# Optimization experiments

Measured on AMD Instinct MI355X. Metric: run time of the kernel, lower is better.

## Reference

```python
import jax, jax.numpy as jnp
import numpy as np
import math

IN_FEATURES = 3072
PADDED = 4096  # next power of two
ACT_BITS = 8
LN_EPS = 1e-6


def hadamard_transform(x):
    """Normalized fast Walsh-Hadamard transform along last dim (power of 2)."""
    n = x.shape[-1]
    m = n.bit_length() - 1  # log2(n)
    shape = x.shape
    y = x.reshape(shape[:-1] + (2,) * m)
    for ax in range(len(shape) - 1, len(shape) - 1 + m):
        a = jnp.take(y, 0, axis=ax)
        b = jnp.take(y, 1, axis=ax)
        y = jnp.stack([a + b, a - b], axis=ax)
    return y.reshape(shape) / jnp.sqrt(jnp.asarray(n, x.dtype))


def activation_quant(x, bits=ACT_BITS):
    """Per-token absmax int-b quant with STE (BitNet style)."""
    qb = 2 ** (bits - 1) - 1  # 127
    scale = qb / jnp.clip(jnp.max(jnp.abs(x), axis=-1, keepdims=True), 1e-5)
    q = jnp.clip(jnp.round(x * scale), -qb - 1, qb) / scale
    return x + jax.lax.stop_gradient(q - x)


def weight_quant(w):
    """Ternary absmean weight quant with STE (as in training path)."""
    scale = jnp.clip(jnp.mean(jnp.abs(w)), 1e-5)
    q = jnp.clip(jnp.round(w / scale), -1.0, 1.0) * scale
    return w + jax.lax.stop_gradient(q - w)


def layer_norm(x, gamma, beta, eps=LN_EPS):
    mu = jnp.mean(x, axis=-1, keepdims=True)
    var = jnp.mean(jnp.square(x - mu), axis=-1, keepdims=True)
    return (x - mu) * jax.lax.rsqrt(var + eps) * gamma + beta


def setup_inputs() -> dict:
    key = jax.random.key(0)
    k1, k2 = jax.random.split(key)
    x = jax.random.normal(k1, (4, 2048, IN_FEATURES), dtype=jnp.float32)
    ln_gamma = jnp.ones((IN_FEATURES,), dtype=jnp.float32)
    ln_beta = jnp.zeros((IN_FEATURES,), dtype=jnp.float32)
    weight = jax.random.normal(k2, (4096, PADDED), dtype=jnp.float32) * 0.02
    return {"x": x, "ln_gamma": ln_gamma, "ln_beta": ln_beta, "weight": weight}


def reference(x, ln_gamma, ln_beta, weight):
    x_norm = layer_norm(x, ln_gamma, ln_beta)
    pad = PADDED - IN_FEATURES
    x_pad = jnp.pad(x_norm, ((0, 0), (0, 0), (0, pad)))
    x_had = hadamard_transform(x_pad)
    x_q = activation_quant(x_had)
    w_q = weight_quant(weight)
    # F.linear: x @ W^T
    out = jnp.einsum('bsd,od->bso', x_q, w_q)
    return out
```

## Files before the change

kernel.cpp:

```cpp
#include <hip/hip_runtime.h>
#include <stdint.h>

#define TOKENS 8192
#define IN_F   3072
#define PAD_F  4096
#define N_OUT  4096
#define K_DIM  4096

using i32x4 = __attribute__((ext_vector_type(4))) int;

#define Q_OFF    0
#define WQ_OFF   33554432
#define AINV_OFF 50331648
#define PART_OFF 50364416
#define WSC_OFF  50380800

__device__ __forceinline__ void gload_lds16(const void* g, void* l) {
    __builtin_amdgcn_global_load_lds(
        (__attribute__((address_space(1))) void*)(void*)g,
        (__attribute__((address_space(3))) void*)l,
        16, 0, 0);
}

__global__ __launch_bounds__(256) void k_wabs(const float* __restrict__ w,
                                              float* __restrict__ partial) {
    int tid = threadIdx.x;
    const float4* w4 = (const float4*)(w + (size_t)blockIdx.x * 4096);
    float s = 0.f;
#pragma unroll
    for (int i = 0; i < 4; ++i) {
        float4 v = w4[tid + i * 256];
        s += fabsf(v.x) + fabsf(v.y) + fabsf(v.z) + fabsf(v.w);
    }
#pragma unroll
    for (int o = 32; o > 0; o >>= 1) s += __shfl_xor(s, o);
    __shared__ float rb[4];
    if ((tid & 63) == 0) rb[tid >> 6] = s;
    __syncthreads();
    if (tid == 0) partial[blockIdx.x] = rb[0] + rb[1] + rb[2] + rb[3];
}

__global__ __launch_bounds__(256) void k_wscale(const float* __restrict__ partial,
                                                float* __restrict__ wsp) {
    int tid = threadIdx.x;
    float s = 0.f;
#pragma unroll
    for (int i = 0; i < 16; ++i) s += partial[tid + i * 256];
#pragma unroll
    for (int o = 32; o > 0; o >>= 1) s += __shfl_xor(s, o);
    __shared__ float rb[4];
    if ((tid & 63) == 0) rb[tid >> 6] = s;
    __syncthreads();
    if (tid == 0)
        wsp[0] = fmaxf((rb[0] + rb[1] + rb[2] + rb[3]) * (1.0f / 16777216.0f), 1e-5f);
}

__global__ __launch_bounds__(256) void k_wquant(const float* __restrict__ w,
                                                const float* __restrict__ wsp,
                                                unsigned int* __restrict__ wq) {
    int idx = blockIdx.x * 256 + threadIdx.x;
    float ws = wsp[0];
    float4 v = ((const float4*)w)[idx];
    int a = (int)rintf(v.x / ws); a = max(-1, min(1, a));
    int b = (int)rintf(v.y / ws); b = max(-1, min(1, b));
    int c = (int)rintf(v.z / ws); c = max(-1, min(1, c));
    int d = (int)rintf(v.w / ws); d = max(-1, min(1, d));
    unsigned int p = (unsigned)(a & 255) | ((unsigned)(b & 255) << 8) |
                     ((unsigned)(c & 255) << 16) | ((unsigned)(d & 255) << 24);
    wq[idx] = p;
}

__global__ __launch_bounds__(256) void k_lnfwht(const float* __restrict__ x,
                                                const float* __restrict__ gamma,
                                                const float* __restrict__ beta,
                                                signed char* __restrict__ q,
                                                float* __restrict__ ainv) {
    __shared__ float s[PAD_F];
    __shared__ float rb[8];
    int tid = threadIdx.x;
    int lane = tid & 63;
    int t = blockIdx.x;
    const float* xr = x + (size_t)t * IN_F;

    float v[16];
    float sum = 0.f;
#pragma unroll
    for (int i = 0; i < 12; ++i) { v[i] = xr[tid + i * 256]; sum += v[i]; }
    v[12] = v[13] = v[14] = v[15] = 0.f;
#pragma unroll
    for (int o = 32; o > 0; o >>= 1) sum += __shfl_xor(sum, o);
    if ((tid & 63) == 0) rb[tid >> 6] = sum;
    __syncthreads();
    float mu = (rb[0] + rb[1] + rb[2] + rb[3]) * (1.0f / 3072.0f);

    float s2 = 0.f;
#pragma unroll
    for (int i = 0; i < 12; ++i) { float d = v[i] - mu; s2 += d * d; }
#pragma unroll
    for (int o = 32; o > 0; o >>= 1) s2 += __shfl_xor(s2, o);
    if ((tid & 63) == 0) rb[4 + (tid >> 6)] = s2;
    __syncthreads();
    float var = (rb[4] + rb[5] + rb[6] + rb[7]) * (1.0f / 3072.0f);
    float rstd = 1.0f / sqrtf(var + 1e-6f);

#pragma unroll
    for (int i = 0; i < 12; ++i)
        v[i] = (v[i] - mu) * rstd * gamma[tid + i * 256] + beta[tid + i * 256];

#pragma unroll
    for (int b = 1; b < 16; b <<= 1) {
#pragma unroll
        for (int i = 0; i < 16; ++i) {
            if (!(i & b)) {
                float a0 = v[i], b0 = v[i | b];
                v[i] = a0 + b0;
                v[i | b] = a0 - b0;
            }
        }
    }
#pragma unroll
    for (int m = 1; m <= 32; m <<= 1) {
#pragma unroll
        for (int i = 0; i < 16; ++i) {
            float p = __shfl_xor(v[i], m);
            v[i] = (lane & m) ? (p - v[i]) : (v[i] + p);
        }
    }
#pragma unroll
    for (int m = 64; m <= 128; m <<= 1) {
        __syncthreads();
#pragma unroll
        for (int i = 0; i < 16; ++i) s[tid + i * 256] = v[i];
        __syncthreads();
#pragma unroll
        for (int i = 0; i < 16; ++i) {
            float p = s[(tid ^ m) + i * 256];
            v[i] = (tid & m) ? (p - v[i]) : (v[i] + p);
        }
    }

    float mx = 0.f;
#pragma unroll
    for (int i = 0; i < 16; ++i) mx = fmaxf(mx, fabsf(v[i]));
#pragma unroll
    for (int o = 32; o > 0; o >>= 1) mx = fmaxf(mx, __shfl_xor(mx, o));
    __syncthreads();
    if ((tid & 63) == 0) rb[tid >> 6] = mx;
    __syncthreads();
    float amraw = fmaxf(fmaxf(rb[0], rb[1]), fmaxf(rb[2], rb[3]));
    float amax = fmaxf(amraw * (1.0f / 64.0f), 1e-5f);
    float scale = 127.0f / amax;
    if (tid == 0) ainv[t] = amax * (1.0f / 127.0f);

    signed char* qr = q + (size_t)t * PAD_F;
#pragma unroll
    for (int i = 0; i < 16; ++i) {
        int qi = (int)rintf(v[i] * (1.0f / 64.0f) * scale);
        qi = max(-128, min(127, qi));
        qr[tid + i * 256] = (signed char)qi;
    }
}

#define BK 64
#define NT (K_DIM / BK)

__global__ __launch_bounds__(512, 2) void k_gemm(const signed char* __restrict__ Aq,
                                                 const signed char* __restrict__ Wq,
                                                 const float* __restrict__ ainv,
                                                 const float* __restrict__ wsp,
                                                 float* __restrict__ out) {
    __shared__ signed char sA[4][256 * BK];
    __shared__ signed char sB[4][256 * BK];

    int tid = threadIdx.x;
    int lane = tid & 63, wid = tid >> 6;

    int bid = blockIdx.x;
    int xcd = bid & 7, li = bid >> 3;
    int bmb = xcd * 4 + (li & 3);
    int bnb = li >> 2;
    size_t bm0 = (size_t)bmb * 256, bn0 = (size_t)bnb * 256;

    int wm = wid >> 2, wn = wid & 3;
    int lrow = lane & 15, hi = lane >> 4;

    int srow = lane >> 2;
    int schunk = (lane & 3) ^ ((lane >> 3) & 3);
    const signed char* gA = Aq + (bm0 + (size_t)(wid * 32 + srow)) * K_DIM + schunk * 16;
    const signed char* gB = Wq + (bn0 + (size_t)(wid * 32 + srow)) * K_DIM + schunk * 16;

    i32x4 acc[8][4];
#pragma unroll
    for (int m = 0; m < 8; ++m)
#pragma unroll
        for (int n = 0; n < 4; ++n) acc[m][n] = (i32x4){0, 0, 0, 0};

    int kx = hi ^ ((lane >> 1) & 3);
    int abase = (wm * 128 + lrow) * 4 + kx;
    int bbase = (wn * 64 + lrow) * 4 + kx;

    auto STAGE = [&](int b, int t) {
        size_t k0 = (size_t)t * BK;
        gload_lds16(gA + k0, &sA[b][(wid * 32) * BK]);
        gload_lds16(gA + k0 + (size_t)16 * K_DIM, &sA[b][(wid * 32 + 16) * BK]);
        gload_lds16(gB + k0, &sB[b][(wid * 32) * BK]);
        gload_lds16(gB + k0 + (size_t)16 * K_DIM, &sB[b][(wid * 32 + 16) * BK]);
    };

    auto COMPUTE = [&](int b) {
        const i32x4* va = (const i32x4*)&sA[b][0];
        const i32x4* vb = (const i32x4*)&sB[b][0];
        i32x4 af[8], bf[4];
#pragma unroll
        for (int m = 0; m < 8; ++m) af[m] = va[abase + m * 64];
#pragma unroll
        for (int n = 0; n < 4; ++n) bf[n] = vb[bbase + n * 64];
        __builtin_amdgcn_s_setprio(1);
#pragma unroll
        for (int m = 0; m < 8; ++m)
#pragma unroll
            for (int n = 0; n < 4; ++n)
                acc[m][n] = __builtin_amdgcn_mfma_i32_16x16x64_i8(af[m], bf[n], acc[m][n], 0, 0, 0);
        __builtin_amdgcn_s_setprio(0);
    };

    STAGE(0, 0);
    STAGE(1, 1);
    STAGE(2, 2);

#pragma unroll 1
    for (int t = 0; t < NT - 3; ++t) {
        STAGE((t + 3) & 3, t + 3);
        asm volatile("s_waitcnt vmcnt(12)" ::: "memory");
        __builtin_amdgcn_s_barrier();
        __builtin_amdgcn_sched_barrier(0);
        COMPUTE(t & 3);
        __builtin_amdgcn_sched_barrier(0);
        __builtin_amdgcn_s_barrier();
    }
    asm volatile("s_waitcnt vmcnt(8)" ::: "memory");
    __builtin_amdgcn_s_barrier();
    __builtin_amdgcn_sched_barrier(0);
    COMPUTE((NT - 3) & 3);
    asm volatile("s_waitcnt vmcnt(4)" ::: "memory");
    __builtin_amdgcn_s_barrier();
    __builtin_amdgcn_sched_barrier(0);
    COMPUTE((NT - 2) & 3);
    asm volatile("s_waitcnt vmcnt(0)" ::: "memory");
    __builtin_amdgcn_s_barrier();
    __builtin_amdgcn_sched_barrier(0);
    COMPUTE((NT - 1) & 3);

    float wsc = wsp[0];
#pragma unroll
    for (int m = 0; m < 8; ++m) {
        size_t row0 = bm0 + wm * 128 + m * 16 + hi * 4;
#pragma unroll
        for (int r = 0; r < 4; ++r) {
            size_t row = row0 + r;
            float sa = wsc * ainv[row];
#pragma unroll
            for (int n = 0; n < 4; ++n) {
                size_t col = bn0 + wn * 64 + n * 16 + lrow;
                out[row * N_OUT + col] = (float)acc[m][n][r] * sa;
            }
        }
    }
}

extern "C" void kernel_launch(void* const* d_in, const int* in_sizes, int n_in,
                              void* d_out, int out_size, void* d_ws, size_t ws_size,
                              hipStream_t stream) {
    const float* x     = (const float*)d_in[0];
    const float* gamma = (const float*)d_in[1];
    const float* beta  = (const float*)d_in[2];
    const float* w     = (const float*)d_in[3];
    float* out = (float*)d_out;
    char* ws = (char*)d_ws;

    signed char* q   = (signed char*)(ws + Q_OFF);
    signed char* wq  = (signed char*)(ws + WQ_OFF);
    float* ainv      = (float*)(ws + AINV_OFF);
    float* partial   = (float*)(ws + PART_OFF);
    float* wsp       = (float*)(ws + WSC_OFF);

    k_wabs<<<dim3(4096), dim3(256), 0, stream>>>(w, partial);
    k_wscale<<<dim3(1), dim3(256), 0, stream>>>(partial, wsp);
    k_wquant<<<dim3(16384), dim3(256), 0, stream>>>(w, wsp, (unsigned int*)wq);
    k_lnfwht<<<dim3(TOKENS), dim3(256), 0, stream>>>(x, gamma, beta, q, ainv);
    k_gemm<<<dim3(512), dim3(512), 0, stream>>>(q, wq, ainv, wsp, out);
}
```

Baseline: 244.8 us.

## Switch GEMM to 32x32x32 int8 MFMA with register double-buffered LDS fragments

Replaces the 16x16x64 int8 MFMA tiling with 32x32x32 instructions, which cuts the number of LDS fragment loads per output. It also adds register double-buffering: fragments for the next K-tile are read from LDS while the current tile's MFMAs run, and one barrier per iteration is removed. The loop is unrolled by two to alternate the fragment buffers, and the epilogue is remapped to the 32x32 accumulator layout. This raises register pressure and tightens the waitcnt and barrier ordering, so correctness depends on the reduced sync still protecting LDS buffer reuse.

```diff
diff --git a/kernel.cpp b/kernel.cpp
--- a/kernel.cpp
+++ b/kernel.cpp
@@ -7,7 +7,8 @@
 #define N_OUT  4096
 #define K_DIM  4096
 
-using i32x4 = __attribute__((ext_vector_type(4))) int;
+using i32x4  = __attribute__((ext_vector_type(4))) int;
+using i32x16 = __attribute__((ext_vector_type(16))) int;
 
 #define Q_OFF    0
 #define WQ_OFF   33554432
@@ -182,22 +183,24 @@
     size_t bm0 = (size_t)bmb * 256, bn0 = (size_t)bnb * 256;
 
     int wm = wid >> 2, wn = wid & 3;
-    int lrow = lane & 15, hi = lane >> 4;
 
     int srow = lane >> 2;
     int schunk = (lane & 3) ^ ((lane >> 3) & 3);
     const signed char* gA = Aq + (bm0 + (size_t)(wid * 32 + srow)) * K_DIM + schunk * 16;
     const signed char* gB = Wq + (bn0 + (size_t)(wid * 32 + srow)) * K_DIM + schunk * 16;
 
-    i32x4 acc[8][4];
-#pragma unroll
-    for (int m = 0; m < 8; ++m)
-#pragma unroll
-        for (int n = 0; n < 4; ++n) acc[m][n] = (i32x4){0, 0, 0, 0};
-
-    int kx = hi ^ ((lane >> 1) & 3);
-    int abase = (wm * 128 + lrow) * 4 + kx;
-    int bbase = (wn * 64 + lrow) * 4 + kx;
+    int r32 = lane & 31, ks32 = lane >> 5;
+    int kq = ks32 ^ ((r32 >> 1) & 3);
+    int abase = (wm * 128 + r32) * 4;
+    int bbase = (wn * 64 + r32) * 4;
+
+    i32x16 acc[4][2];
+#pragma unroll
+    for (int mf = 0; mf < 4; ++mf)
+#pragma unroll
+        for (int nf = 0; nf < 2; ++nf) acc[mf][nf] = (i32x16)(0);
+
+    i32x4 afA[2][4], bfA[2][2], afB[2][4], bfB[2][2];
 
     auto STAGE = [&](int b, int t) {
         size_t k0 = (size_t)t * BK;
@@ -207,65 +210,98 @@
         gload_lds16(gB + k0 + (size_t)16 * K_DIM, &sB[b][(wid * 32 + 16) * BK]);
     };
 
-    auto COMPUTE = [&](int b) {
-        const i32x4* va = (const i32x4*)&sA[b][0];
-        const i32x4* vb = (const i32x4*)&sB[b][0];
-        i32x4 af[8], bf[4];
-#pragma unroll
-        for (int m = 0; m < 8; ++m) af[m] = va[abase + m * 64];
-#pragma unroll
-        for (int n = 0; n < 4; ++n) bf[n] = vb[bbase + n * 64];
-        __builtin_amdgcn_s_setprio(1);
-#pragma unroll
-        for (int m = 0; m < 8; ++m)
-#pragma unroll
-            for (int n = 0; n < 4; ++n)
-                acc[m][n] = __builtin_amdgcn_mfma_i32_16x16x64_i8(af[m], bf[n], acc[m][n], 0, 0, 0);
-        __builtin_amdgcn_s_setprio(0);
-    };
+#define LOADF(B, AF, BF) do {                                           \
+    const i32x4* va = (const i32x4*)&sA[B][0];                          \
+    const i32x4* vb = (const i32x4*)&sB[B][0];                          \
+    _Pragma("unroll")                                                   \
+    for (int ks = 0; ks < 2; ++ks) {                                    \
+        int kx = (ks << 1) ^ kq;                                        \
+        _Pragma("unroll")                                               \
+        for (int mf = 0; mf < 4; ++mf) AF[ks][mf] = va[abase + mf * 128 + kx]; \
+        _Pragma("unroll")                                               \
+        for (int nf = 0; nf < 2; ++nf) BF[ks][nf] = vb[bbase + nf * 128 + kx]; \
+    }                                                                   \
+} while (0)
+
+#define COMPUTE(AF, BF) do {                                            \
+    __builtin_amdgcn_s_setprio(1);                                      \
+    _Pragma("unroll")                                                   \
+    for (int ks = 0; ks < 2; ++ks)                                      \
+        _Pragma("unroll")                                               \
+        for (int mf = 0; mf < 4; ++mf)                                  \
+            _Pragma("unroll")                                           \
+            for (int nf = 0; nf < 2; ++nf)                              \
+                acc[mf][nf] = __builtin_amdgcn_mfma_i32_32x32x32_i8(    \
+                    AF[ks][mf], BF[ks][nf], acc[mf][nf], 0, 0, 0);      \
+    __builtin_amdgcn_s_setprio(0);                                      \
+} while (0)
+
+#define BODY(T, AFC, BFC, AFN, BFN) do {                                \
+    STAGE((T + 3) & 3, T + 3);                                          \
+    asm volatile("s_waitcnt vmcnt(8)" ::: "memory");                    \
+    __builtin_amdgcn_sched_barrier(0);                                  \
+    __builtin_amdgcn_s_barrier();                                       \
+    __builtin_amdgcn_sched_barrier(0);                                  \
+    LOADF((T + 1) & 3, AFN, BFN);                                       \
+    COMPUTE(AFC, BFC);                                                  \
+    asm volatile("s_waitcnt lgkmcnt(0)" ::: "memory");                  \
+    __builtin_amdgcn_sched_barrier(0);                                  \
+} while (0)
 
     STAGE(0, 0);
     STAGE(1, 1);
     STAGE(2, 2);
+    asm volatile("s_waitcnt vmcnt(8)" ::: "memory");
+    __builtin_amdgcn_sched_barrier(0);
+    __builtin_amdgcn_s_barrier();
+    __builtin_amdgcn_sched_barrier(0);
+    LOADF(0, afA, bfA);
+    asm volatile("s_waitcnt lgkmcnt(0)" ::: "memory");
+    __builtin_amdgcn_sched_barrier(0);
 
 #pragma unroll 1
-    for (int t = 0; t < NT - 3; ++t) {
-        STAGE((t + 3) & 3, t + 3);
-        asm volatile("s_waitcnt vmcnt(12)" ::: "memory");
-        __builtin_amdgcn_s_barrier();
-        __builtin_amdgcn_sched_barrier(0);
-        COMPUTE(t & 3);
-        __builtin_amdgcn_sched_barrier(0);
-        __builtin_amdgcn_s_barrier();
-    }
-    asm volatile("s_waitcnt vmcnt(8)" ::: "memory");
+    for (int t = 0; t < NT - 4; t += 2) {
+        BODY(t, afA, bfA, afB, bfB);
+        BODY(t + 1, afB, bfB, afA, bfA);
+    }
+    BODY(NT - 4, afA, bfA, afB, bfB);
+    asm volatile("s_waitcnt vmcnt(4)" ::: "memory");
+    __builtin_amdgcn_sched_barrier(0);
     __builtin_amdgcn_s_barrier();
     __builtin_amdgcn_sched_barrier(0);
-    COMPUTE((NT - 3) & 3);
-    asm volatile("s_waitcnt vmcnt(4)" ::: "memory");
+    LOADF(2, afA, bfA);
+    COMPUTE(afB, bfB);
+    asm volatile("s_waitcnt lgkmcnt(0)" ::: "memory");
+    __builtin_amdgcn_sched_barrier(0);
+    asm volatile("s_waitcnt vmcnt(0)" ::: "memory");
+    __builtin_amdgcn_sched_barrier(0);
     __builtin_amdgcn_s_barrier();
     __builtin_amdgcn_sched_barrier(0);
-    COMPUTE((NT - 2) & 3);
-    asm volatile("s_waitcnt vmcnt(0)" ::: "memory");
-    __builtin_amdgcn_s_barrier();
-    __builtin_amdgcn_sched_barrier(0);
-    COMPUTE((NT - 1) & 3);
+    LOADF(3, afB, bfB);
+    COMPUTE(afA, bfA);
+    asm volatile("s_waitcnt lgkmcnt(0)" ::: "memory");
+    __builtin_amdgcn_sched_barrier(0);
+    COMPUTE(afB, bfB);
 
     float wsc = wsp[0];
-#pragma unroll
-    for (int m = 0; m < 8; ++m) {
-        size_t row0 = bm0 + wm * 128 + m * 16 + hi * 4;
-#pragma unroll
-        for (int r = 0; r < 4; ++r) {
-            size_t row = row0 + r;
+    int c31 = lane & 31, hi2 = lane >> 5;
+#pragma unroll
+    for (int mf = 0; mf < 4; ++mf) {
+        size_t rowb = bm0 + wm * 128 + mf * 32 + 4 * hi2;
+#pragma unroll
+        for (int reg = 0; reg < 16; ++reg) {
+            size_t row = rowb + (reg & 3) + 8 * (reg >> 2);
             float sa = wsc * ainv[row];
 #pragma unroll
-            for (int n = 0; n < 4; ++n) {
-                size_t col = bn0 + wn * 64 + n * 16 + lrow;
-                out[row * N_OUT + col] = (float)acc[m][n][r] * sa;
+            for (int nf = 0; nf < 2; ++nf) {
+                size_t col = bn0 + wn * 64 + nf * 32 + c31;
+                out[row * N_OUT + col] = (float)acc[mf][nf][reg] * sa;
             }
         }
     }
+#undef LOADF
+#undef COMPUTE
+#undef BODY
 }
 
 extern "C" void kernel_launch(void* const* d_in, const int* in_sizes, int n_in,
```

Measured after the change: 231.2 us. 1.06x faster.
